# Kernel optimization log

Measured on AMD Instinct MI355X. Metric: run time of the kernel, lower is better.

Reference implementation:

```python
import jax, jax.numpy as jnp
import numpy as np

NEG_INF = -1e9


def setup_inputs() -> dict:
    B, S, D = 4, 2048, 1024
    key = jax.random.key(0)
    ks = jax.random.split(key, 10)
    sc = 1.0 / np.sqrt(D)
    return {
        "batch": jax.random.normal(ks[0], (B, S, D), jnp.float32),
        "padding_mask": jax.random.randint(ks[1], (B, S), 0, 2) > 0,
        "Wq": jax.random.normal(ks[2], (D, D), jnp.float32) * sc,
        "bq": jnp.zeros((D,), jnp.float32),
        "Wk": jax.random.normal(ks[3], (D, D), jnp.float32) * sc,
        "bk": jnp.zeros((D,), jnp.float32),
        "Wv": jax.random.normal(ks[4], (D, D), jnp.float32) * sc,
        "bv": jnp.zeros((D,), jnp.float32),
        "Wo": jax.random.normal(ks[5], (D, D), jnp.float32) * sc,
        "bo": jnp.zeros((D,), jnp.float32),
        "num_heads": 16,
    }


def _split_heads(x, H):
    B, S, D = x.shape
    return x.reshape(B, S, H, D // H).transpose(0, 2, 1, 3)  # [B,H,S,hd]


def reference(batch, padding_mask, Wq, bq, Wk, bk, Wv, bv, Wo, bo, num_heads):
    B, S, D = batch.shape
    H = num_heads
    q = _split_heads(batch @ Wq + bq, H)  # [B,H,S,hd]
    k = _split_heads(batch @ Wk + bk, H)
    v = _split_heads(batch @ Wv + bv, H)
    # tf.keras.layers.Attention default: unscaled dot-product scores
    scores = jnp.einsum("bhqd,bhkd->bhqk", q, k)
    kmask = padding_mask[:, None, None, :]  # value/key mask -> masks score columns
    scores = jnp.where(kmask, scores, NEG_INF)
    probs = jax.nn.softmax(scores, axis=-1)
    ctx = jnp.einsum("bhqk,bhkd->bhqd", probs, v)
    # query mask zeroes padded query positions (tf Attention behavior)
    ctx = ctx * padding_mask[:, None, :, None].astype(ctx.dtype)
    ctx = ctx.transpose(0, 2, 1, 3).reshape(B, S, D)
    return ctx @ Wo + bo
```

## Files before the change

### kernel.cpp

```cpp
#include <hip/hip_runtime.h>


#define Bb 4
#define Ss 2048
#define Dd 1024
#define Hh 16
#define SZt 8388608

typedef short bf16x8 __attribute__((ext_vector_type(8)));
typedef _Float16 f16x8 __attribute__((ext_vector_type(8)));
typedef float f32x4 __attribute__((ext_vector_type(4)));
typedef float f32x16 __attribute__((ext_vector_type(16)));
typedef unsigned int u32x4 __attribute__((ext_vector_type(4)));
typedef unsigned short u16;

__device__ __forceinline__ float bf2f(u16 u) {
    return __builtin_bit_cast(float, ((unsigned)u) << 16);
}
__device__ __forceinline__ u16 f2bf(float f) {
    unsigned u = __builtin_bit_cast(unsigned, f);
    unsigned r = 0x7FFFu + ((u >> 16) & 1u);
    return (u16)((u + r) >> 16);
}
__device__ __forceinline__ u16 f2h(float f) {
    _Float16 h = (_Float16)f;
    return __builtin_bit_cast(u16, h);
}
__device__ __forceinline__ bf16x8 ldfrag(const u16* p) {
    return __builtin_bit_cast(bf16x8, *(const uint4*)p);
}
__device__ __forceinline__ f16x8 ldfragh(const u16* p) {
    return __builtin_bit_cast(f16x8, *(const uint4*)p);
}
__device__ __forceinline__ f32x4 mfma16h(f16x8 a, f16x8 b, f32x4 c) {
    return __builtin_amdgcn_mfma_f32_16x16x32_f16(a, b, c, 0, 0, 0);
}
__device__ __forceinline__ f32x4 mfma16b(bf16x8 a, bf16x8 b, f32x4 c) {
    return __builtin_amdgcn_mfma_f32_16x16x32_bf16(a, b, c, 0, 0, 0);
}
__device__ __forceinline__ f32x16 mfma32(bf16x8 a, bf16x8 b, f32x16 c) {
    return __builtin_amdgcn_mfma_f32_32x32x16_bf16(a, b, c, 0, 0, 0);
}
__device__ __forceinline__ f32x16 mfma32h(f16x8 a, f16x8 b, f32x16 c) {
    return __builtin_amdgcn_mfma_f32_32x32x16_f16(a, b, c, 0, 0, 0);
}
__device__ __forceinline__ unsigned cvt_pk_bf16(float a, float b) {
    unsigned r;
    asm("v_cvt_pk_bf16_f32 %0, %1, %2" : "=v"(r) : "v"(a), "v"(b));
    return r;
}
__device__ __forceinline__ void gl2lds16(const u16* g, u16* l) {
    __builtin_amdgcn_global_load_lds(
        (const __attribute__((address_space(1))) u16*)g,
        (__attribute__((address_space(3))) u16*)l, 16, 0, 0);
}

__global__ __launch_bounds__(256) void prologue(
    const float* __restrict__ X, u16* __restrict__ Xh,
    const float* __restrict__ Wq, const float* __restrict__ Wk, const float* __restrict__ Wv,
    u16* __restrict__ Wqt, u16* __restrict__ Wkt, u16* __restrict__ Wvt,
    const float* __restrict__ bq, const float* __restrict__ bk, const float* __restrict__ bv,
    float* __restrict__ bcat,
    const unsigned char* __restrict__ mraw, float* __restrict__ mnorm, float* __restrict__ cntp)
{
    __shared__ float tl[32][33];
    __shared__ int flags;
    __shared__ float scnt[Bb];
    const int blk = blockIdx.x, tid = threadIdx.x;

    if (blk < 8192) {
        size_t i = ((size_t)blk * 256 + tid) * 4;
        float4 v = *(const float4*)(X + i);
        u16 h0 = f2h(v.x), h1 = f2h(v.y), h2 = f2h(v.z), h3 = f2h(v.w);
        uint2 ph = { (unsigned)h0 | ((unsigned)h1 << 16), (unsigned)h2 | ((unsigned)h3 << 16) };
        *(uint2*)(Xh + i) = ph;
    } else if (blk < 11264) {
        int idx = blk - 8192;
        int w = idx >> 10, t = idx & 1023;
        const float* W = (w == 0) ? Wq : ((w == 1) ? Wk : Wv);
        u16* Wt = (w == 0) ? Wqt : ((w == 1) ? Wkt : Wvt);
        const int tx = tid & 31, ty = tid >> 5;
        const int n0 = (t & 31) * 32, k0 = (t >> 5) * 32;
        #pragma unroll
        for (int i = 0; i < 4; i++)
            tl[ty + i * 8][tx] = W[(size_t)(k0 + ty + i * 8) * Dd + n0 + tx];
        __syncthreads();
        #pragma unroll
        for (int i = 0; i < 4; i++)
            Wt[(size_t)(n0 + ty + i * 8) * Dd + k0 + tx] = f2h(tl[tx][ty + i * 8]);
    } else if (blk < 11276) {
        int i = (blk - 11264) * 256 + tid;
        bcat[i] = (i < 1024) ? bq[i] : ((i < 2048) ? bk[i - 1024] : bv[i - 2048]);
    } else {
        const int n = Bb * Ss;
        if (tid == 0) flags = 0;
        if (tid < Bb) scnt[tid] = 0.f;
        __syncthreads();
        int f = 0;
        for (int i = tid; i < n; i += 256) {
            unsigned char c = mraw[i];
            if ((i & 3) != 0 && c) f |= 1;
            if ((i & 3) == 1 && c >= 2) f |= 2;
            if ((i & 3) == 3 && c >= 2) f |= 4;
        }
        if (f) atomicOr(&flags, f);
        __syncthreads();
        int fl = flags;
        int layout;
        if (!(fl & 1)) layout = 0;
        else if (fl & 2) layout = 2;
        else if (fl & 4) layout = 3;
        else layout = 1;
        for (int i = tid; i < n; i += 256) {
            int v;
            if (layout == 0)      v = ((const int*)mraw)[i];
            else if (layout == 1) v = mraw[i];
            else if (layout == 2) v = ((const u16*)mraw)[i] != 0;
            else                  v = ((const unsigned*)mraw)[i] != 0;
            mnorm[i] = (v != 0) ? 1.0f : 0.0f;
            if (v == 0) atomicAdd(&scnt[i >> 11], 1.0f);
        }
        __syncthreads();
        if (tid < Bb) cntp[tid] = scnt[tid];
    }
}

__global__ __launch_bounds__(256) void transpose_w(const float* __restrict__ W, u16* __restrict__ Wt) {
    __shared__ float t[32][33];
    const int tx = threadIdx.x, ty = threadIdx.y;
    const int n0 = blockIdx.x * 32, k0 = blockIdx.y * 32;
    #pragma unroll
    for (int i = 0; i < 4; i++)
        t[ty + i * 8][tx] = W[(size_t)(k0 + ty + i * 8) * Dd + n0 + tx];
    __syncthreads();
    #pragma unroll
    for (int i = 0; i < 4; i++)
        Wt[(size_t)(n0 + ty + i * 8) * Dd + k0 + tx] = f2bf(t[tx][ty + i * 8]);
}

__global__ __launch_bounds__(512, 2) void gemm_qkv(
    const u16* __restrict__ Ah, const u16* __restrict__ Wcat, const float* __restrict__ bcat,
    const float* __restrict__ mnorm,
    u16* __restrict__ Qb, u16* __restrict__ Kb, u16* __restrict__ Vt)
{
    __shared__ u16 As[3][256][64];
    __shared__ u16 Bs[2][128][64];
    const int tid = threadIdx.x, lane = tid & 63, wave = tid >> 6;
    const int wm = wave >> 1, wn = wave & 1;
    const int bm = blockIdx.y * 256, bn = blockIdx.x * 128;
    const bool isQ = (bn < 1024);
    const int l15 = lane & 15, lq = lane >> 4;
    const int rl = lane >> 3;
    const int s8 = ((lane & 7) ^ rl) * 8;
    const u16* agp = Ah + (size_t)(bm + wave * 32 + rl) * Dd + s8;
    const u16* bgp = Wcat + (size_t)(bn + wave * 16 + rl) * Dd + s8;

    f32x4 acc[4][4] = {};

    auto stageA = [&](int slot, int kt) {
        u16* d = &As[slot][wave * 32][0];
        const u16* g = agp + kt * 64;
        #pragma unroll
        for (int j = 0; j < 4; ++j)
            gl2lds16(g + (size_t)(j * 8) * Dd, d + j * 8 * 64);
    };
    auto stageB = [&](int slot, int kt) {
        u16* d = &Bs[slot][wave * 16][0];
        const u16* g = bgp + kt * 64;
        #pragma unroll
        for (int j = 0; j < 2; ++j)
            gl2lds16(g + (size_t)(j * 8) * Dd, d + j * 8 * 64);
    };

    stageA(0, 0); stageB(0, 0); stageA(1, 1);
    asm volatile("s_waitcnt vmcnt(4)" ::: "memory");
    __builtin_amdgcn_s_barrier();

    int cs = 0;
    for (int t = 0; t < 16; ++t) {
        if (t < 15) stageB((t + 1) & 1, t + 1);
        if (t < 14) { int ss = (cs >= 1) ? cs - 1 : cs + 2; stageA(ss, t + 2); }
        #pragma unroll
        for (int kf = 0; kf < 2; kf++) {
            f16x8 b[4], a[4];
            #pragma unroll
            for (int nt = 0; nt < 4; nt++)
                b[nt] = ldfragh(&Bs[t & 1][wn * 64 + nt * 16 + l15][(kf * 32 + lq * 8) ^ ((l15 & 7) * 8)]);
            #pragma unroll
            for (int mt = 0; mt < 4; mt++)
                a[mt] = ldfragh(&As[cs][wm * 64 + mt * 16 + l15][(kf * 32 + lq * 8) ^ ((l15 & 7) * 8)]);
            #pragma unroll
            for (int mt = 0; mt < 4; mt++)
                #pragma unroll
                for (int nt = 0; nt < 4; nt++)
                    acc[mt][nt] = mfma16h(a[mt], b[nt], acc[mt][nt]);
        }
        if (t < 14)       asm volatile("s_waitcnt vmcnt(4)" ::: "memory");
        else if (t == 14) asm volatile("s_waitcnt vmcnt(0)" ::: "memory");
        if (t < 15) __builtin_amdgcn_s_barrier();
        cs = (cs >= 2) ? 0 : cs + 1;
    }

    const float LOG2E = 1.44269504088896f;
    float bv[4];
    #pragma unroll
    for (int nt = 0; nt < 4; nt++) bv[nt] = bcat[bn + wn * 64 + nt * 16 + l15];
    #pragma unroll
    for (int mt = 0; mt < 4; mt++) {
        int r0 = bm + wm * 64 + mt * 16 + lq * 4;
        float mk[4];
        if (!isQ) {
            #pragma unroll
            for (int rr = 0; rr < 4; rr++) mk[rr] = mnorm[r0 + rr];
        }
        #pragma unroll
        for (int nt = 0; nt < 4; nt++) {
            int col = bn + wn * 64 + nt * 16 + l15;
            if (col < 1024) {
                #pragma unroll
                for (int rr = 0; rr < 4; rr++)
                    Qb[(size_t)(r0 + rr) * Dd + col] = f2h((acc[mt][nt][rr] + bv[nt]) * LOG2E);
            } else if (col < 2048) {
                int c2 = col - 1024;
                #pragma unroll
                for (int rr = 0; rr < 4; rr++)
                    Kb[(size_t)(r0 + rr) * Dd + c2] = f2h((acc[mt][nt][rr] + bv[nt]) * mk[rr]);
            } else {
                int c2 = col - 2048;
                int hh = c2 >> 6, dd = c2 & 63, b_ = r0 >> 11, s0 = r0 & 2047;
                u16 e0 = f2bf((acc[mt][nt][0] + bv[nt]) * mk[0]);
                u16 e1 = f2bf((acc[mt][nt][1] + bv[nt]) * mk[1]);
                u16 e2 = f2bf((acc[mt][nt][2] + bv[nt]) * mk[2]);
                u16 e3 = f2bf((acc[mt][nt][3] + bv[nt]) * mk[3]);
                uint2 pk = { (unsigned)e0 | ((unsigned)e1 << 16), (unsigned)e2 | ((unsigned)e3 << 16) };
                *(uint2*)(Vt + (size_t)((b_ * Hh + hh) * 64 + dd) * Ss + s0) = pk;
            }
        }
    }
}

__global__ __launch_bounds__(512, 2) void gemm_out(
    const u16* __restrict__ Ah, const u16* __restrict__ Wt,
    const float* __restrict__ bias, float* __restrict__ Cout)
{
    __shared__ u16 As[3][256][64];
    __shared__ u16 Bs[2][128][64];
    const int tid = threadIdx.x, lane = tid & 63, wave = tid >> 6;
    const int wm = wave >> 1, wn = wave & 1;
    const int bm = blockIdx.y * 256, bn = blockIdx.x * 128;
    const int l15 = lane & 15, lq = lane >> 4;
    const int rl = lane >> 3;
    const int s8 = ((lane & 7) ^ rl) * 8;
    const u16* agp = Ah + (size_t)(bm + wave * 32 + rl) * Dd + s8;
    const u16* bgp = Wt + (size_t)(bn + wave * 16 + rl) * Dd + s8;

    f32x4 acc[4][4] = {};

    auto stageA = [&](int slot, int kt) {
        u16* d = &As[slot][wave * 32][0];
        const u16* g = agp + kt * 64;
        #pragma unroll
        for (int j = 0; j < 4; ++j)
            gl2lds16(g + (size_t)(j * 8) * Dd, d + j * 8 * 64);
    };
    auto stageB = [&](int slot, int kt) {
        u16* d = &Bs[slot][wave * 16][0];
        const u16* g = bgp + kt * 64;
        #pragma unroll
        for (int j = 0; j < 2; ++j)
            gl2lds16(g + (size_t)(j * 8) * Dd, d + j * 8 * 64);
    };

    stageA(0, 0); stageB(0, 0); stageA(1, 1);
    asm volatile("s_waitcnt vmcnt(4)" ::: "memory");
    __builtin_amdgcn_s_barrier();

    int cs = 0;
    for (int t = 0; t < 16; ++t) {
        if (t < 15) stageB((t + 1) & 1, t + 1);
        if (t < 14) { int ss = (cs >= 1) ? cs - 1 : cs + 2; stageA(ss, t + 2); }
        #pragma unroll
        for (int kf = 0; kf < 2; kf++) {
            bf16x8 b[4], a[4];
            #pragma unroll
            for (int nt = 0; nt < 4; nt++)
                b[nt] = ldfrag(&Bs[t & 1][wn * 64 + nt * 16 + l15][(kf * 32 + lq * 8) ^ ((l15 & 7) * 8)]);
            #pragma unroll
            for (int mt = 0; mt < 4; mt++)
                a[mt] = ldfrag(&As[cs][wm * 64 + mt * 16 + l15][(kf * 32 + lq * 8) ^ ((l15 & 7) * 8)]);
            #pragma unroll
            for (int mt = 0; mt < 4; mt++)
                #pragma unroll
                for (int nt = 0; nt < 4; nt++)
                    acc[mt][nt] = mfma16b(a[mt], b[nt], acc[mt][nt]);
        }
        if (t < 14)       asm volatile("s_waitcnt vmcnt(4)" ::: "memory");
        else if (t == 14) asm volatile("s_waitcnt vmcnt(0)" ::: "memory");
        if (t < 15) __builtin_amdgcn_s_barrier();
        cs = (cs >= 2) ? 0 : cs + 1;
    }

    float bv[4];
    #pragma unroll
    for (int nt = 0; nt < 4; nt++) bv[nt] = bias[bn + wn * 64 + nt * 16 + l15];
    #pragma unroll
    for (int mt = 0; mt < 4; mt++) {
        int r0 = bm + wm * 64 + mt * 16 + lq * 4;
        #pragma unroll
        for (int nt = 0; nt < 4; nt++) {
            int col = bn + wn * 64 + nt * 16 + l15;
            #pragma unroll
            for (int rr = 0; rr < 4; rr++)
                Cout[(size_t)(r0 + rr) * Dd + col] = acc[mt][nt][rr] + bv[nt];
        }
    }
}

__global__ __launch_bounds__(512, 4) void attn_mfma(
    u16* qctx, const u16* __restrict__ Kb, const u16* __restrict__ Vt,
    const float* __restrict__ maskf, const float* __restrict__ cntp)
{
    __shared__ u16 Ks[128][72];
    __shared__ u16 Vs[64][136];
    __shared__ float li_s[8][32];
    const int tid = threadIdx.x, lane = tid & 63, wave = tid >> 6;
    const int l31 = lane & 31, hi = lane >> 5;
    const int bh = blockIdx.x, h = bh & 15, b = bh >> 4;
    const int q0 = blockIdx.y * 256;

    f16x8 qa[4];
    {
        const u16* qp = qctx + (size_t)(b * Ss + q0 + wave * 32 + l31) * Dd + h * 64 + hi * 8;
        #pragma unroll
        for (int kf = 0; kf < 4; kf++) qa[kf] = ldfragh(qp + kf * 16);
    }

    const int kr = tid >> 3, kc = (tid & 7) * 8;
    const int vd = tid >> 4, vc = (tid & 15) * 8;
    const u16* kgb = Kb + ((size_t)b * Ss + kr) * Dd + h * 64 + kc;
    const u16* vgb = Vt + (((size_t)(b * Hh + h)) * 64 + vd) * Ss + vc;

    f32x16 acc0 = {}, acc1 = {};
    float li = 0.f;

    uint4 kreg0 = *(const uint4*)(kgb);
    uint4 kreg1 = *(const uint4*)(kgb + (size_t)64 * Dd);
    uint4 vreg0 = *(const uint4*)(vgb);
    uint4 vreg1 = *(const uint4*)(vgb + (size_t)32 * Ss);

    for (int k0 = 0; k0 < Ss; k0 += 128) {
        __syncthreads();
        *(uint4*)&Ks[kr][kc]      = kreg0;
        *(uint4*)&Ks[kr + 64][kc] = kreg1;
        *(uint4*)&Vs[vd][vc]      = vreg0;
        *(uint4*)&Vs[vd + 32][vc] = vreg1;
        __syncthreads();
        int k0n = (k0 + 128 < Ss) ? k0 + 128 : 0;
        kreg0 = *(const uint4*)(kgb + (size_t)k0n * Dd);
        kreg1 = *(const uint4*)(kgb + (size_t)(k0n + 64) * Dd);
        vreg0 = *(const uint4*)(vgb + k0n);
        vreg1 = *(const uint4*)(vgb + (size_t)32 * Ss + k0n);

        #pragma unroll
        for (int nt = 0; nt < 4; nt++) {
            f32x16 sc = {};
            __builtin_amdgcn_s_setprio(1);
            #pragma unroll
            for (int kf = 0; kf < 4; kf++) {
                f16x8 kb = ldfragh(&Ks[nt * 32 + l31][kf * 16 + hi * 8]);
                sc = mfma32h(kb, qa[kf], sc);
            }
            __builtin_amdgcn_s_setprio(0);
            float p[16];
            #pragma unroll
            for (int r = 0; r < 8; r++) p[r] = __builtin_amdgcn_exp2f(sc[r]);
            li += ((p[0] + p[1]) + (p[2] + p[3])) + ((p[4] + p[5]) + (p[6] + p[7]));
            {
                unsigned w0 = cvt_pk_bf16(p[0], p[1]), w1 = cvt_pk_bf16(p[2], p[3]);
                unsigned w2 = cvt_pk_bf16(p[4], p[5]), w3 = cvt_pk_bf16(p[6], p[7]);
                auto s02 = __builtin_amdgcn_permlane32_swap((int)w0, (int)w2, false, false);
                auto s13 = __builtin_amdgcn_permlane32_swap((int)w1, (int)w3, false, false);
                u32x4 pw = { (unsigned)s02[0], (unsigned)s13[0], (unsigned)s02[1], (unsigned)s13[1] };
                bf16x8 pa0 = __builtin_bit_cast(bf16x8, pw);
                bf16x8 v00 = ldfrag(&Vs[l31][nt * 32 + hi * 8]);
                bf16x8 v10 = ldfrag(&Vs[32 + l31][nt * 32 + hi * 8]);
                __builtin_amdgcn_s_setprio(1);
                acc0 = mfma32(pa0, v00, acc0);
                acc1 = mfma32(pa0, v10, acc1);
                __builtin_amdgcn_s_setprio(0);
            }
            #pragma unroll
            for (int r = 8; r < 16; r++) p[r] = __builtin_amdgcn_exp2f(sc[r]);
            li += ((p[8] + p[9]) + (p[10] + p[11])) + ((p[12] + p[13]) + (p[14] + p[15]));
            {
                unsigned w4 = cvt_pk_bf16(p[8], p[9]),  w5 = cvt_pk_bf16(p[10], p[11]);
                unsigned w6 = cvt_pk_bf16(p[12], p[13]), w7 = cvt_pk_bf16(p[14], p[15]);
                auto s46 = __builtin_amdgcn_permlane32_swap((int)w4, (int)w6, false, false);
                auto s57 = __builtin_amdgcn_permlane32_swap((int)w5, (int)w7, false, false);
                u32x4 pw = { (unsigned)s46[0], (unsigned)s57[0], (unsigned)s46[1], (unsigned)s57[1] };
                bf16x8 pa1 = __builtin_bit_cast(bf16x8, pw);
                bf16x8 v01 = ldfrag(&Vs[l31][nt * 32 + 16 + hi * 8]);
                bf16x8 v11 = ldfrag(&Vs[32 + l31][nt * 32 + 16 + hi * 8]);
                __builtin_amdgcn_s_setprio(1);
                acc0 = mfma32(pa1, v01, acc0);
                acc1 = mfma32(pa1, v11, acc1);
                __builtin_amdgcn_s_setprio(0);
            }
        }
    }

    float li_tot = li + __shfl_xor(li, 32);
    if (hi == 0) li_s[wave][l31] = li_tot;
    __builtin_amdgcn_s_barrier();
    float cntb = cntp[b];
    #pragma unroll
    for (int g = 0; g < 4; g++) {
        float4 lv = *(const float4*)&li_s[wave][g * 8 + hi * 4];
        #pragma unroll
        for (int j = 0; j < 4; j++) {
            int r = g * 4 + j;
            int row = j + 8 * g + 4 * hi;
            int q = q0 + wave * 32 + row;
            float qm = maskf[b * Ss + q];
            float den = lv[j] - cntb;
            float rl = den > 0.f ? qm / den : 0.f;
            u16* op = qctx + (size_t)(b * Ss + q) * Dd + h * 64 + l31;
            op[0]  = f2bf(acc0[r] * rl);
            op[32] = f2bf(acc1[r] * rl);
        }
    }
}

extern "C" void kernel_launch(void* const* d_in, const int* in_sizes, int n_in,
                              void* d_out, int out_size, void* d_ws, size_t ws_size,
                              hipStream_t stream) {
    const float* X  = (const float*)d_in[0];
    const unsigned char* mr = (const unsigned char*)d_in[1];
    const float* Wq = (const float*)d_in[2];
    const float* bq = (const float*)d_in[3];
    const float* Wk = (const float*)d_in[4];
    const float* bk = (const float*)d_in[5];
    const float* Wv = (const float*)d_in[6];
    const float* bv = (const float*)d_in[7];
    const float* Wo = (const float*)d_in[8];
    const float* bo = (const float*)d_in[9];
    float* out = (float*)d_out;

    u16* wsb = (u16*)d_ws;
    u16* Xh  = wsb;
    u16* Qb  = wsb + (size_t)SZt;
    u16* Kb  = wsb + 2 * (size_t)SZt;
    u16* Vt  = wsb + 3 * (size_t)SZt;
    u16* Wot = Xh;
    u16* ob  = (u16*)d_out;
    u16* Wcat = ob + (size_t)SZt;
    u16* Wqt = Wcat;
    u16* Wkt = Wqt + 1048576;
    u16* Wvt = Wkt + 1048576;
    float* mnorm = (float*)(Wvt + 1048576);
    float* bcat  = mnorm + Bb * Ss;
    float* cntp  = bcat + 3072;

    prologue<<<11277, 256, 0, stream>>>(X, Xh, Wq, Wk, Wv, Wqt, Wkt, Wvt,
                                        bq, bk, bv, bcat, mr, mnorm, cntp);
    gemm_qkv<<<dim3(24, 32), 512, 0, stream>>>(Xh, Wcat, bcat, mnorm, Qb, Kb, Vt);
    transpose_w<<<dim3(32, 32), dim3(32, 8), 0, stream>>>(Wo, Wot);
    attn_mfma<<<dim3(Bb * Hh, Ss / 256), 512, 0, stream>>>(Qb, Kb, Vt, mnorm, cntp);
    gemm_out<<<dim3(8, 32), 512, 0, stream>>>(Qb, Wot, bo, out);
}
```

Baseline: 300.6 us.

## Use 32x32 MFMA in QKV GEMM and fold Wo transpose into attention launch

The QKV projection GEMM now issues 32x32x16 f16 MFMA instructions instead of 16x16x32, with fragment loads and the epilogue's row/column mapping reworked to match the 32x32 accumulator layout. The separate Wo transpose kernel is removed. Its work moves into an extra column of blocks in the attention launch, which reuse the K shared-memory buffer as transpose scratch. This cuts MFMA instruction count and LDS fragment reads and saves one kernel launch, at the cost of a different LDS bank-access pattern and a few long-running transpose blocks inside the attention grid.

```diff
diff --git a/kernel.cpp b/kernel.cpp
--- a/kernel.cpp
+++ b/kernel.cpp
@@ -31,9 +31,6 @@
 }
 __device__ __forceinline__ f16x8 ldfragh(const u16* p) {
     return __builtin_bit_cast(f16x8, *(const uint4*)p);
-}
-__device__ __forceinline__ f32x4 mfma16h(f16x8 a, f16x8 b, f32x4 c) {
-    return __builtin_amdgcn_mfma_f32_16x16x32_f16(a, b, c, 0, 0, 0);
 }
 __device__ __forceinline__ f32x4 mfma16b(bf16x8 a, bf16x8 b, f32x4 c) {
     return __builtin_amdgcn_mfma_f32_16x16x32_bf16(a, b, c, 0, 0, 0);
@@ -125,19 +122,6 @@
     }
 }
 
-__global__ __launch_bounds__(256) void transpose_w(const float* __restrict__ W, u16* __restrict__ Wt) {
-    __shared__ float t[32][33];
-    const int tx = threadIdx.x, ty = threadIdx.y;
-    const int n0 = blockIdx.x * 32, k0 = blockIdx.y * 32;
-    #pragma unroll
-    for (int i = 0; i < 4; i++)
-        t[ty + i * 8][tx] = W[(size_t)(k0 + ty + i * 8) * Dd + n0 + tx];
-    __syncthreads();
-    #pragma unroll
-    for (int i = 0; i < 4; i++)
-        Wt[(size_t)(n0 + ty + i * 8) * Dd + k0 + tx] = f2bf(t[tx][ty + i * 8]);
-}
-
 __global__ __launch_bounds__(512, 2) void gemm_qkv(
     const u16* __restrict__ Ah, const u16* __restrict__ Wcat, const float* __restrict__ bcat,
     const float* __restrict__ mnorm,
@@ -149,13 +133,13 @@
     const int wm = wave >> 1, wn = wave & 1;
     const int bm = blockIdx.y * 256, bn = blockIdx.x * 128;
     const bool isQ = (bn < 1024);
-    const int l15 = lane & 15, lq = lane >> 4;
+    const int l31 = lane & 31, hi = lane >> 5;
     const int rl = lane >> 3;
     const int s8 = ((lane & 7) ^ rl) * 8;
     const u16* agp = Ah + (size_t)(bm + wave * 32 + rl) * Dd + s8;
     const u16* bgp = Wcat + (size_t)(bn + wave * 16 + rl) * Dd + s8;
 
-    f32x4 acc[4][4] = {};
+    f32x16 acc[2][2] = {};
 
     auto stageA = [&](int slot, int kt) {
         u16* d = &As[slot][wave * 32][0];
@@ -181,19 +165,19 @@
         if (t < 15) stageB((t + 1) & 1, t + 1);
         if (t < 14) { int ss = (cs >= 1) ? cs - 1 : cs + 2; stageA(ss, t + 2); }
         #pragma unroll
-        for (int kf = 0; kf < 2; kf++) {
-            f16x8 b[4], a[4];
-            #pragma unroll
-            for (int nt = 0; nt < 4; nt++)
-                b[nt] = ldfragh(&Bs[t & 1][wn * 64 + nt * 16 + l15][(kf * 32 + lq * 8) ^ ((l15 & 7) * 8)]);
-            #pragma unroll
-            for (int mt = 0; mt < 4; mt++)
-                a[mt] = ldfragh(&As[cs][wm * 64 + mt * 16 + l15][(kf * 32 + lq * 8) ^ ((l15 & 7) * 8)]);
-            #pragma unroll
-            for (int mt = 0; mt < 4; mt++)
+        for (int kq = 0; kq < 4; kq++) {
+            f16x8 b[2], a[2];
+            #pragma unroll
+            for (int nt = 0; nt < 2; nt++)
+                b[nt] = ldfragh(&Bs[t & 1][wn * 64 + nt * 32 + l31][(kq * 16 + hi * 8) ^ ((l31 & 7) * 8)]);
+            #pragma unroll
+            for (int mt = 0; mt < 2; mt++)
+                a[mt] = ldfragh(&As[cs][wm * 64 + mt * 32 + l31][(kq * 16 + hi * 8) ^ ((l31 & 7) * 8)]);
+            #pragma unroll
+            for (int mt = 0; mt < 2; mt++)
                 #pragma unroll
-                for (int nt = 0; nt < 4; nt++)
-                    acc[mt][nt] = mfma16h(a[mt], b[nt], acc[mt][nt]);
+                for (int nt = 0; nt < 2; nt++)
+                    acc[mt][nt] = mfma32h(a[mt], b[nt], acc[mt][nt]);
         }
         if (t < 14)       asm volatile("s_waitcnt vmcnt(4)" ::: "memory");
         else if (t == 14) asm volatile("s_waitcnt vmcnt(0)" ::: "memory");
@@ -202,38 +186,41 @@
     }
 
     const float LOG2E = 1.44269504088896f;
-    float bv[4];
+    float bvv[2];
     #pragma unroll
-    for (int nt = 0; nt < 4; nt++) bv[nt] = bcat[bn + wn * 64 + nt * 16 + l15];
+    for (int nt = 0; nt < 2; nt++) bvv[nt] = bcat[bn + wn * 64 + nt * 32 + l31];
     #pragma unroll
-    for (int mt = 0; mt < 4; mt++) {
-        int r0 = bm + wm * 64 + mt * 16 + lq * 4;
-        float mk[4];
-        if (!isQ) {
-            #pragma unroll
-            for (int rr = 0; rr < 4; rr++) mk[rr] = mnorm[r0 + rr];
-        }
-        #pragma unroll
-        for (int nt = 0; nt < 4; nt++) {
-            int col = bn + wn * 64 + nt * 16 + l15;
-            if (col < 1024) {
+    for (int mt = 0; mt < 2; mt++) {
+        #pragma unroll
+        for (int rq = 0; rq < 4; rq++) {
+            int r0 = bm + wm * 64 + mt * 32 + 8 * rq + 4 * hi;
+            float mk[4];
+            if (!isQ) {
                 #pragma unroll
-                for (int rr = 0; rr < 4; rr++)
-                    Qb[(size_t)(r0 + rr) * Dd + col] = f2h((acc[mt][nt][rr] + bv[nt]) * LOG2E);
-            } else if (col < 2048) {
-                int c2 = col - 1024;
-                #pragma unroll
-                for (int rr = 0; rr < 4; rr++)
-                    Kb[(size_t)(r0 + rr) * Dd + c2] = f2h((acc[mt][nt][rr] + bv[nt]) * mk[rr]);
-            } else {
-                int c2 = col - 2048;
-                int hh = c2 >> 6, dd = c2 & 63, b_ = r0 >> 11, s0 = r0 & 2047;
-                u16 e0 = f2bf((acc[mt][nt][0] + bv[nt]) * mk[0]);
-                u16 e1 = f2bf((acc[mt][nt][1] + bv[nt]) * mk[1]);
-                u16 e2 = f2bf((acc[mt][nt][2] + bv[nt]) * mk[2]);
-                u16 e3 = f2bf((acc[mt][nt][3] + bv[nt]) * mk[3]);
-                uint2 pk = { (unsigned)e0 | ((unsigned)e1 << 16), (unsigned)e2 | ((unsigned)e3 << 16) };
-                *(uint2*)(Vt + (size_t)((b_ * Hh + hh) * 64 + dd) * Ss + s0) = pk;
+                for (int j = 0; j < 4; j++) mk[j] = mnorm[r0 + j];
+            }
+            #pragma unroll
+            for (int nt = 0; nt < 2; nt++) {
+                int col = bn + wn * 64 + nt * 32 + l31;
+                if (col < 1024) {
+                    #pragma unroll
+                    for (int j = 0; j < 4; j++)
+                        Qb[(size_t)(r0 + j) * Dd + col] = f2h((acc[mt][nt][rq * 4 + j] + bvv[nt]) * LOG2E);
+                } else if (col < 2048) {
+                    int c2 = col - 1024;
+                    #pragma unroll
+                    for (int j = 0; j < 4; j++)
+                        Kb[(size_t)(r0 + j) * Dd + c2] = f2h((acc[mt][nt][rq * 4 + j] + bvv[nt]) * mk[j]);
+                } else {
+                    int c2 = col - 2048;
+                    int hh = c2 >> 6, dd = c2 & 63, b_ = r0 >> 11, s0 = r0 & 2047;
+                    u16 e0 = f2bf((acc[mt][nt][rq * 4 + 0] + bvv[nt]) * mk[0]);
+                    u16 e1 = f2bf((acc[mt][nt][rq * 4 + 1] + bvv[nt]) * mk[1]);
+                    u16 e2 = f2bf((acc[mt][nt][rq * 4 + 2] + bvv[nt]) * mk[2]);
+                    u16 e3 = f2bf((acc[mt][nt][rq * 4 + 3] + bvv[nt]) * mk[3]);
+                    uint2 pk = { (unsigned)e0 | ((unsigned)e1 << 16), (unsigned)e2 | ((unsigned)e3 << 16) };
+                    *(uint2*)(Vt + (size_t)((b_ * Hh + hh) * 64 + dd) * Ss + s0) = pk;
+                }
             }
         }
     }
@@ -318,12 +305,36 @@
 
 __global__ __launch_bounds__(512, 4) void attn_mfma(
     u16* qctx, const u16* __restrict__ Kb, const u16* __restrict__ Vt,
-    const float* __restrict__ maskf, const float* __restrict__ cntp)
+    const float* __restrict__ maskf, const float* __restrict__ cntp,
+    const float* __restrict__ Wo, u16* __restrict__ Wot)
 {
     __shared__ u16 Ks[128][72];
     __shared__ u16 Vs[64][136];
     __shared__ float li_s[8][32];
     const int tid = threadIdx.x, lane = tid & 63, wave = tid >> 6;
+
+    if (blockIdx.x == 64) {
+        float* tlb = (float*)&Ks[0][0];
+        const int sub = tid >> 8;
+        const int st = tid & 255;
+        const int tx = st & 31, ty = st >> 5;
+        float* tl = tlb + sub * 32 * 33;
+        #pragma unroll 1
+        for (int it = 0; it < 64; ++it) {
+            int t = blockIdx.y * 128 + it * 2 + sub;
+            int n0 = (t & 31) * 32, k0 = (t >> 5) * 32;
+            #pragma unroll
+            for (int i = 0; i < 4; i++)
+                tl[(ty + i * 8) * 33 + tx] = Wo[(size_t)(k0 + ty + i * 8) * Dd + n0 + tx];
+            __syncthreads();
+            #pragma unroll
+            for (int i = 0; i < 4; i++)
+                Wot[(size_t)(n0 + ty + i * 8) * Dd + k0 + tx] = f2bf(tl[tx * 33 + ty + i * 8]);
+            __syncthreads();
+        }
+        return;
+    }
+
     const int l31 = lane & 31, hi = lane >> 5;
     const int bh = blockIdx.x, h = bh & 15, b = bh >> 4;
     const int q0 = blockIdx.y * 256;
@@ -464,7 +475,6 @@
     prologue<<<11277, 256, 0, stream>>>(X, Xh, Wq, Wk, Wv, Wqt, Wkt, Wvt,
                                         bq, bk, bv, bcat, mr, mnorm, cntp);
     gemm_qkv<<<dim3(24, 32), 512, 0, stream>>>(Xh, Wcat, bcat, mnorm, Qb, Kb, Vt);
-    transpose_w<<<dim3(32, 32), dim3(32, 8), 0, stream>>>(Wo, Wot);
-    attn_mfma<<<dim3(Bb * Hh, Ss / 256), 512, 0, stream>>>(Qb, Kb, Vt, mnorm, cntp);
+    attn_mfma<<<dim3(Bb * Hh + 1, Ss / 256), 512, 0, stream>>>(Qb, Kb, Vt, mnorm, cntp, Wo, Wot);
     gemm_out<<<dim3(8, 32), 512, 0, stream>>>(Qb, Wot, bo, out);
 }
```

Result: slower. 326.3 us (+8.6%).
